# Performance work log

Hardware: AMD Instinct MI355X
Metric: run time of the kernel (lower is better)

The kernel has to match this reference:

```python
import jax, jax.numpy as jnp
import numpy as np

A = 100.0
EPSILON = 0.1
NUM_NEG = 10
N = 100000
DIM = 64


def setup_inputs() -> dict:
    key = jax.random.key(0)
    k1, k2, k3 = jax.random.split(key, 3)
    x = jax.random.normal(k1, (N, DIM), dtype=jnp.float32)
    u_idx = jax.random.randint(k2, (N * NUM_NEG,), 0, N)
    v_idx = jax.random.randint(k3, (N * NUM_NEG,), 0, N)
    return {"x": x, "u_idx": u_idx, "v_idx": v_idx}


def reference(x, u_idx, v_idx):
    # Minkowski signature vector J = [-1, 1, ..., 1]
    J = jnp.ones((DIM,), dtype=x.dtype).at[0].set(-1.0)

    xu = x[u_idx]                      # (E, dim) gather
    xv = x[v_idx]                      # (E, dim) gather

    inner = jnp.sum(xu * xv * J, axis=-1)                 # (E,) Minkowski inner product
    inner = jnp.minimum(inner, -1.0 - 1e-7)               # clamp(max=-1-1e-7)
    dist = jnp.arccosh(-inner)                            # hyperbolic distance

    mask = dist < EPSILON                                 # data-dependent activity mask
    delta = jnp.where(mask, EPSILON - dist, 0.0)          # zero out inactive pairs

    energy = 0.5 * A * jnp.sum(delta ** 2) / NUM_NEG

    denom = jnp.sqrt(inner ** 2 - 1.0)
    force_mag = A * delta / NUM_NEG                       # already zero where inactive
    factor = jnp.where(mask, -(force_mag / (denom + 1e-9)), 0.0)[:, None]  # (E,1)

    grad = jnp.zeros_like(x)
    grad = grad.at[u_idx].add(factor * (xv * J))          # scatter-add over pairs
    grad = grad.at[v_idx].add(factor * (xu * J))
    return energy, grad
```

## Files before the change

kernel.cpp:

```cpp
#include <hip/hip_runtime.h>

#define EPS_F 0.1f
#define A_F 100.0f
#define NUMNEG_F 10.0f
#define EXP_EPS 1.1051709f
#define CAP 64
#define BATCH 16
#define NBLOCKS 4096

__global__ __launch_bounds__(256) void fill_kernel(
    const int* __restrict__ u_idx, const int* __restrict__ v_idx,
    int* __restrict__ counts, int* __restrict__ entries,
    float* __restrict__ out, int out_n, int E)
{
    const int tid = blockIdx.x * blockDim.x + threadIdx.x;
    const int nthreads = gridDim.x * blockDim.x;

    float4* o4 = (float4*)out;
    const int n4 = out_n >> 2;
    for (int i = tid; i < n4; i += nthreads) o4[i] = float4{0.f, 0.f, 0.f, 0.f};
    if (tid == 0)
        for (int i = n4 * 4; i < out_n; i++) out[i] = 0.f;

    for (int i = tid; i < E; i += nthreads) {
        const int u = u_idx[i];
        const int slot = atomicAdd(&counts[u], 1);
        if (slot < CAP) entries[(size_t)u * CAP + slot] = v_idx[i];
    }
}

__device__ __forceinline__ float red2(float a, float b, int dist, bool sel) {
    const float fa = a + __shfl_xor(a, dist, 64);
    const float fb = b + __shfl_xor(b, dist, 64);
    return sel ? fb : fa;
}

#define PROCESS_BATCH(xuj, vs, xv, bn, gacc)                                   \
    do {                                                                       \
        float p[BATCH];                                                        \
        _Pragma("unroll")                                                      \
        for (int k = 0; k < BATCH; k++) p[k] = (xuj) * (xv)[k];                \
        float q0 = red2(p[0], p[8],  32, m32);                                 \
        float q1 = red2(p[1], p[9],  32, m32);                                 \
        float q2 = red2(p[2], p[10], 32, m32);                                 \
        float q3 = red2(p[3], p[11], 32, m32);                                 \
        float q4 = red2(p[4], p[12], 32, m32);                                 \
        float q5 = red2(p[5], p[13], 32, m32);                                 \
        float q6 = red2(p[6], p[14], 32, m32);                                 \
        float q7 = red2(p[7], p[15], 32, m32);                                 \
        float r0 = red2(q0, q4, 16, m16);                                      \
        float r1 = red2(q1, q5, 16, m16);                                      \
        float r2 = red2(q2, q6, 16, m16);                                      \
        float r3 = red2(q3, q7, 16, m16);                                      \
        float s0 = red2(r0, r2, 8, m8);                                        \
        float s1 = red2(r1, r3, 8, m8);                                        \
        float t0 = red2(s0, s1, 4, m4);                                        \
        t0 += __shfl_xor(t0, 2, 64);                                           \
        t0 += __shfl_xor(t0, 1, 64);                                           \
        const float inner = fminf(t0, -1.0f - 1e-7f);                          \
        const float sq    = __builtin_amdgcn_sqrtf(fmaf(inner, inner, -1.0f)); \
        const float tt    = sq - inner;                                        \
        const bool  act   = (tt < EXP_EPS) & (e4 < (bn));                      \
        const float dist  = __logf(tt);                                        \
        const float delta = act ? (EPS_F - dist) : 0.0f;                       \
        eacc = fmaf(delta, delta, eacc);                                       \
        const float factor = (-(A_F / NUMNEG_F)) * delta *                     \
                             __builtin_amdgcn_rcpf(sq + 1e-9f);                \
        const unsigned long long ball = __ballot(act);                         \
        _Pragma("unroll")                                                      \
        for (int k = 0; k < BATCH; k++) {                                      \
            if ((ball >> (4 * k)) & 1ull) {                                    \
                const float fk = __uint_as_float(                              \
                    __builtin_amdgcn_readlane(__float_as_uint(factor), 4 * k));\
                unsafeAtomicAdd(&grad[(size_t)(vs)[k] * 64 + lane], fk * (xuj));\
                (gacc) = fmaf(fk, (xv)[k], (gacc));                            \
            }                                                                  \
        }                                                                      \
    } while (0)

__global__ __launch_bounds__(256) void node_kernel(
    const float* __restrict__ x,
    const int* __restrict__ counts,
    const int* __restrict__ entries,
    float* __restrict__ out,
    float* __restrict__ block_energy,
    int N)
{
    const int lane = threadIdx.x & 63;
    const int wib  = threadIdx.x >> 6;
    const int wave = (blockIdx.x * blockDim.x + threadIdx.x) >> 6;
    const int nwaves = (gridDim.x * blockDim.x) >> 6;
    const float sign = (lane == 0) ? -1.0f : 1.0f;
    float* __restrict__ grad = out + 1;

    const bool m32 = (lane & 32) != 0;
    const bool m16 = (lane & 16) != 0;
    const bool m8  = (lane & 8)  != 0;
    const bool m4  = (lane & 4)  != 0;
    const int  e4  = lane >> 2;

    float eacc = 0.0f;

    int uA = wave * 2;
    const int stride = nwaves * 2;
    int degA = 0, myvA = 0, degB = 0, myvB = 0;
    if (uA < N)     { degA = counts[uA];     myvA = entries[(size_t)uA * CAP + lane]; }
    if (uA + 1 < N) { degB = counts[uA + 1]; myvB = entries[(size_t)(uA + 1) * CAP + lane]; }

    while (uA < N) {
        const int uB = uA + 1;
        const int bnA = min(degA, BATCH);
        const int bnB = min(degB, BATCH);
        const int myvA_c = myvA, myvB_c = myvB;

        const float xujA = x[(size_t)uA * 64 + lane] * sign;
        const float xujB = (uB < N) ? x[(size_t)uB * 64 + lane] * sign : 0.0f;

        int vsA[BATCH], vsB[BATCH];
        float xvA[BATCH], xvB[BATCH];
        #pragma unroll
        for (int k = 0; k < BATCH; k++) {
            if (k < bnA) {
                vsA[k] = __builtin_amdgcn_readlane(myvA_c, k);
                xvA[k] = x[(size_t)vsA[k] * 64 + lane];
            } else { vsA[k] = 0; xvA[k] = 0.0f; }
        }
        #pragma unroll
        for (int k = 0; k < BATCH; k++) {
            if (k < bnB) {
                vsB[k] = __builtin_amdgcn_readlane(myvB_c, k);
                xvB[k] = x[(size_t)vsB[k] * 64 + lane];
            } else { vsB[k] = 0; xvB[k] = 0.0f; }
        }

        const int uAn = uA + stride;
        int degA2 = 0, myvA2 = 0, degB2 = 0, myvB2 = 0;
        if (uAn < N)     { degA2 = counts[uAn];     myvA2 = entries[(size_t)uAn * CAP + lane]; }
        if (uAn + 1 < N) { degB2 = counts[uAn + 1]; myvB2 = entries[(size_t)(uAn + 1) * CAP + lane]; }

        float gaccA = 0.0f, gaccB = 0.0f;
        PROCESS_BATCH(xujA, vsA, xvA, bnA, gaccA);
        if (bnA > 0) unsafeAtomicAdd(&grad[(size_t)uA * 64 + lane], gaccA * sign);
        PROCESS_BATCH(xujB, vsB, xvB, bnB, gaccB);
        if (bnB > 0) unsafeAtomicAdd(&grad[(size_t)uB * 64 + lane], gaccB * sign);

        uA = uAn; degA = degA2; myvA = myvA2; degB = degB2; myvB = myvB2;
    }

    for (int u = wave; u < N; u += nwaves) {
        const int deg = counts[u];
        if (deg <= BATCH) continue;
        const int deg_c = min(deg, CAP);
        const int myv = entries[(size_t)u * CAP + lane];
        const float xuj = x[(size_t)u * 64 + lane] * sign;
        float gacc = 0.0f;
        for (int k0 = BATCH; k0 < deg_c; k0 += BATCH) {
            const int bn = min(BATCH, deg_c - k0);
            int vs[BATCH]; float xv[BATCH];
            #pragma unroll
            for (int k = 0; k < BATCH; k++) {
                if (k < bn) {
                    vs[k] = __builtin_amdgcn_readlane(myv, k0 + k);
                    xv[k] = x[(size_t)vs[k] * 64 + lane];
                } else { vs[k] = 0; xv[k] = 0.0f; }
            }
            PROCESS_BATCH(xuj, vs, xv, bn, gacc);
        }
        unsafeAtomicAdd(&grad[(size_t)u * 64 + lane], gacc * sign);
    }

    #pragma unroll
    for (int off = 32; off >= 1; off >>= 1) eacc += __shfl_xor(eacc, off, 64);
    __shared__ float se[4];
    if (lane == 0) se[wib] = eacc * 0.25f;
    __syncthreads();
    if (threadIdx.x == 0)
        block_energy[blockIdx.x] = se[0] + se[1] + se[2] + se[3];
}

__global__ __launch_bounds__(256) void energy_reduce_kernel(
    const float* __restrict__ block_energy, float* __restrict__ out, int n)
{
    const int lane = threadIdx.x & 63;
    const int wib  = threadIdx.x >> 6;
    float s = 0.0f;
    for (int i = threadIdx.x; i < n; i += 256) s += block_energy[i];
    #pragma unroll
    for (int off = 32; off >= 1; off >>= 1) s += __shfl_xor(s, off, 64);
    __shared__ float se[4];
    if (lane == 0) se[wib] = s;
    __syncthreads();
    if (threadIdx.x == 0)
        out[0] = (se[0] + se[1] + se[2] + se[3]) * (0.5f * A_F / NUMNEG_F);
}

extern "C" void kernel_launch(void* const* d_in, const int* in_sizes, int n_in,
                              void* d_out, int out_size, void* d_ws, size_t ws_size,
                              hipStream_t stream) {
    const float* x     = (const float*)d_in[0];
    const int*   u_idx = (const int*)d_in[1];
    const int*   v_idx = (const int*)d_in[2];
    float* out = (float*)d_out;
    const int E = in_sizes[1];
    const int N = in_sizes[0] / 64;

    char* ws = (char*)d_ws;
    int*   counts       = (int*)ws;
    int*   entries      = (int*)(ws + (1 << 20));
    float* block_energy = (float*)(ws + (1 << 20) + (size_t)N * CAP * 4 + (1 << 20));

    hipMemsetAsync(counts, 0, (size_t)N * sizeof(int), stream);

    fill_kernel<<<4096, 256, 0, stream>>>(u_idx, v_idx, counts, entries,
                                          out, out_size, E);

    node_kernel<<<NBLOCKS, 256, 0, stream>>>(x, counts, entries, out, block_energy, N);

    energy_reduce_kernel<<<1, 256, 0, stream>>>(block_energy, out, NBLOCKS);
}
```

Baseline: 314.6 us.

## Build CSR adjacency via scan instead of fixed-capacity per-node slots

Replaces the fixed 64-slot per-node neighbor table with a compact CSR adjacency built by histogram, two-level prefix scan, and scatter kernels. The node kernel now processes one node per wave using packed offset/degree metadata, with a fallback path for degrees above 64. This shrinks the adjacency footprint and removes the degree cap, at the cost of extra kernel launches and an additional pass over the edge list.

Result: slower. 321.0 us (+2.0%).

```diff
diff --git a/kernel.cpp b/kernel.cpp
--- a/kernel.cpp
+++ b/kernel.cpp
@@ -4,29 +4,91 @@
 #define A_F 100.0f
 #define NUMNEG_F 10.0f
 #define EXP_EPS 1.1051709f
-#define CAP 64
 #define BATCH 16
 #define NBLOCKS 4096
 
-__global__ __launch_bounds__(256) void fill_kernel(
-    const int* __restrict__ u_idx, const int* __restrict__ v_idx,
-    int* __restrict__ counts, int* __restrict__ entries,
+__global__ __launch_bounds__(256) void hist_kernel(
+    const int* __restrict__ u_idx,
+    int* __restrict__ counts, int* __restrict__ slot,
     float* __restrict__ out, int out_n, int E)
 {
     const int tid = blockIdx.x * blockDim.x + threadIdx.x;
-    const int nthreads = gridDim.x * blockDim.x;
+    const int nth = gridDim.x * blockDim.x;
 
     float4* o4 = (float4*)out;
     const int n4 = out_n >> 2;
-    for (int i = tid; i < n4; i += nthreads) o4[i] = float4{0.f, 0.f, 0.f, 0.f};
+    for (int i = tid; i < n4; i += nth) o4[i] = float4{0.f, 0.f, 0.f, 0.f};
     if (tid == 0)
         for (int i = n4 * 4; i < out_n; i++) out[i] = 0.f;
 
-    for (int i = tid; i < E; i += nthreads) {
-        const int u = u_idx[i];
-        const int slot = atomicAdd(&counts[u], 1);
-        if (slot < CAP) entries[(size_t)u * CAP + slot] = v_idx[i];
-    }
+    for (int e = tid; e < E; e += nth)
+        slot[e] = atomicAdd(&counts[u_idx[e]], 1);
+}
+
+__global__ __launch_bounds__(256) void scan_partial_kernel(
+    const int* __restrict__ counts, int* __restrict__ partials, int N)
+{
+    __shared__ int lds[256];
+    const int i = blockIdx.x * 256 + threadIdx.x;
+    lds[threadIdx.x] = (i < N) ? counts[i] : 0;
+    __syncthreads();
+    for (int off = 128; off >= 1; off >>= 1) {
+        if (threadIdx.x < off) lds[threadIdx.x] += lds[threadIdx.x + off];
+        __syncthreads();
+    }
+    if (threadIdx.x == 0) partials[blockIdx.x] = lds[0];
+}
+
+__global__ __launch_bounds__(64) void scan_bases_kernel(
+    int* __restrict__ partials, int nb)
+{
+    const int lane = threadIdx.x;
+    int carry = 0;
+    for (int base = 0; base < nb; base += 64) {
+        const int i = base + lane;
+        const int orig = (i < nb) ? partials[i] : 0;
+        int v = orig;
+        #pragma unroll
+        for (int off = 1; off < 64; off <<= 1) {
+            const int t = __shfl_up(v, off, 64);
+            if (lane >= off) v += t;
+        }
+        if (i < nb) partials[i] = carry + v - orig;
+        carry += __shfl(v, 63, 64);
+    }
+}
+
+__global__ __launch_bounds__(256) void scan_meta_kernel(
+    const int* __restrict__ counts, const int* __restrict__ bases,
+    int* __restrict__ meta, int N)
+{
+    __shared__ int lds[256];
+    const int t = threadIdx.x;
+    const int i = blockIdx.x * 256 + t;
+    const int deg = (i < N) ? counts[i] : 0;
+    lds[t] = deg;
+    __syncthreads();
+    for (int off = 1; off < 256; off <<= 1) {
+        const int add = (t >= off) ? lds[t - off] : 0;
+        __syncthreads();
+        lds[t] += add;
+        __syncthreads();
+    }
+    if (i < N) {
+        const int excl = lds[t] - deg + bases[blockIdx.x];
+        meta[i] = excl | (deg << 20);
+    }
+}
+
+__global__ __launch_bounds__(256) void scatter_kernel(
+    const int* __restrict__ u_idx, const int* __restrict__ v_idx,
+    const int* __restrict__ slot, const int* __restrict__ meta,
+    int* __restrict__ adj, int E)
+{
+    const int tid = blockIdx.x * blockDim.x + threadIdx.x;
+    const int nth = gridDim.x * blockDim.x;
+    for (int e = tid; e < E; e += nth)
+        adj[(meta[u_idx[e]] & 0xFFFFF) + slot[e]] = v_idx[e];
 }
 
 __device__ __forceinline__ float red2(float a, float b, int dist, bool sel) {
@@ -80,8 +142,8 @@
 
 __global__ __launch_bounds__(256) void node_kernel(
     const float* __restrict__ x,
-    const int* __restrict__ counts,
-    const int* __restrict__ entries,
+    const int* __restrict__ meta,
+    const int* __restrict__ adj,
     float* __restrict__ out,
     float* __restrict__ block_energy,
     int N)
@@ -101,72 +163,55 @@
 
     float eacc = 0.0f;
 
-    int uA = wave * 2;
-    const int stride = nwaves * 2;
-    int degA = 0, myvA = 0, degB = 0, myvB = 0;
-    if (uA < N)     { degA = counts[uA];     myvA = entries[(size_t)uA * CAP + lane]; }
-    if (uA + 1 < N) { degB = counts[uA + 1]; myvB = entries[(size_t)(uA + 1) * CAP + lane]; }
-
-    while (uA < N) {
-        const int uB = uA + 1;
-        const int bnA = min(degA, BATCH);
-        const int bnB = min(degB, BATCH);
-        const int myvA_c = myvA, myvB_c = myvB;
-
-        const float xujA = x[(size_t)uA * 64 + lane] * sign;
-        const float xujB = (uB < N) ? x[(size_t)uB * 64 + lane] * sign : 0.0f;
-
-        int vsA[BATCH], vsB[BATCH];
-        float xvA[BATCH], xvB[BATCH];
-        #pragma unroll
-        for (int k = 0; k < BATCH; k++) {
-            if (k < bnA) {
-                vsA[k] = __builtin_amdgcn_readlane(myvA_c, k);
-                xvA[k] = x[(size_t)vsA[k] * 64 + lane];
-            } else { vsA[k] = 0; xvA[k] = 0.0f; }
-        }
-        #pragma unroll
-        for (int k = 0; k < BATCH; k++) {
-            if (k < bnB) {
-                vsB[k] = __builtin_amdgcn_readlane(myvB_c, k);
-                xvB[k] = x[(size_t)vsB[k] * 64 + lane];
-            } else { vsB[k] = 0; xvB[k] = 0.0f; }
-        }
-
-        const int uAn = uA + stride;
-        int degA2 = 0, myvA2 = 0, degB2 = 0, myvB2 = 0;
-        if (uAn < N)     { degA2 = counts[uAn];     myvA2 = entries[(size_t)uAn * CAP + lane]; }
-        if (uAn + 1 < N) { degB2 = counts[uAn + 1]; myvB2 = entries[(size_t)(uAn + 1) * CAP + lane]; }
-
-        float gaccA = 0.0f, gaccB = 0.0f;
-        PROCESS_BATCH(xujA, vsA, xvA, bnA, gaccA);
-        if (bnA > 0) unsafeAtomicAdd(&grad[(size_t)uA * 64 + lane], gaccA * sign);
-        PROCESS_BATCH(xujB, vsB, xvB, bnB, gaccB);
-        if (bnB > 0) unsafeAtomicAdd(&grad[(size_t)uB * 64 + lane], gaccB * sign);
-
-        uA = uAn; degA = degA2; myvA = myvA2; degB = degB2; myvB = myvB2;
-    }
-
-    for (int u = wave; u < N; u += nwaves) {
-        const int deg = counts[u];
-        if (deg <= BATCH) continue;
-        const int deg_c = min(deg, CAP);
-        const int myv = entries[(size_t)u * CAP + lane];
+    int u = wave;
+    int mu = 0, myv = 0;
+    if (u < N) {
+        mu  = meta[u];
+        myv = adj[(mu & 0xFFFFF) + lane];
+    }
+
+    while (u < N) {
+        const int deg  = mu >> 20;
+        const int base = mu & 0xFFFFF;
+        const int myv_c = myv;
         const float xuj = x[(size_t)u * 64 + lane] * sign;
+
+        const int un = u + nwaves;
+        if (un < N) {
+            mu  = meta[un];
+            myv = adj[(mu & 0xFFFFF) + lane];
+        }
+
         float gacc = 0.0f;
-        for (int k0 = BATCH; k0 < deg_c; k0 += BATCH) {
+        const int deg_c = min(deg, 64);
+        for (int k0 = 0; k0 < deg_c; k0 += BATCH) {
             const int bn = min(BATCH, deg_c - k0);
             int vs[BATCH]; float xv[BATCH];
             #pragma unroll
             for (int k = 0; k < BATCH; k++) {
                 if (k < bn) {
-                    vs[k] = __builtin_amdgcn_readlane(myv, k0 + k);
+                    vs[k] = __builtin_amdgcn_readlane(myv_c, k0 + k);
                     xv[k] = x[(size_t)vs[k] * 64 + lane];
                 } else { vs[k] = 0; xv[k] = 0.0f; }
             }
             PROCESS_BATCH(xuj, vs, xv, bn, gacc);
         }
-        unsafeAtomicAdd(&grad[(size_t)u * 64 + lane], gacc * sign);
+        for (int k0 = 64; k0 < deg; k0 += BATCH) {
+            const int bn = min(BATCH, deg - k0);
+            int vs[BATCH]; float xv[BATCH];
+            #pragma unroll
+            for (int k = 0; k < BATCH; k++) {
+                if (k < bn) {
+                    vs[k] = adj[base + k0 + k];
+                    xv[k] = x[(size_t)vs[k] * 64 + lane];
+                } else { vs[k] = 0; xv[k] = 0.0f; }
+            }
+            PROCESS_BATCH(xuj, vs, xv, bn, gacc);
+        }
+
+        if (deg > 0)
+            unsafeAtomicAdd(&grad[(size_t)u * 64 + lane], gacc * sign);
+        u = un;
     }
 
     #pragma unroll
@@ -203,18 +248,23 @@
     float* out = (float*)d_out;
     const int E = in_sizes[1];
     const int N = in_sizes[0] / 64;
+    const int NB = (N + 255) / 256;
 
     char* ws = (char*)d_ws;
-    int*   counts       = (int*)ws;
-    int*   entries      = (int*)(ws + (1 << 20));
-    float* block_energy = (float*)(ws + (1 << 20) + (size_t)N * CAP * 4 + (1 << 20));
+    int*   counts       = (int*)(ws);
+    int*   slot         = (int*)(ws + (1u << 20));
+    int*   partials     = (int*)(ws + (11u << 19));
+    int*   meta         = (int*)(ws + (6u << 20));
+    int*   adj          = (int*)(ws + (8u << 20));
+    float* block_energy = (float*)(ws + (13u << 20));
 
     hipMemsetAsync(counts, 0, (size_t)N * sizeof(int), stream);
 
-    fill_kernel<<<4096, 256, 0, stream>>>(u_idx, v_idx, counts, entries,
-                                          out, out_size, E);
-
-    node_kernel<<<NBLOCKS, 256, 0, stream>>>(x, counts, entries, out, block_energy, N);
-
+    hist_kernel<<<4096, 256, 0, stream>>>(u_idx, counts, slot, out, out_size, E);
+    scan_partial_kernel<<<NB, 256, 0, stream>>>(counts, partials, N);
+    scan_bases_kernel<<<1, 64, 0, stream>>>(partials, NB);
+    scan_meta_kernel<<<NB, 256, 0, stream>>>(counts, partials, meta, N);
+    scatter_kernel<<<4096, 256, 0, stream>>>(u_idx, v_idx, slot, meta, adj, E);
+    node_kernel<<<NBLOCKS, 256, 0, stream>>>(x, meta, adj, out, block_energy, N);
     energy_reduce_kernel<<<1, 256, 0, stream>>>(block_energy, out, NBLOCKS);
 }
```
